# Optimization experiments

Measured on AMD Instinct MI355X. Metric: run time of the kernel, lower is better.

The kernel has to match this reference:

```python
import jax, jax.numpy as jnp
import numpy as np

MESH_SIZE = 0.01
TEMP = 0.001
T = 4096
HID = (16, 16, 16)


def _triangle_mesh():
    g = np.arange(-1.0, 1.0 + 1e-9, MESH_SIZE, dtype=np.float32)  # 201 pts
    A, B = np.meshgrid(g, g, indexing='ij')  # alpha rows, beta cols
    mask = A >= B                             # Preisach triangle alpha >= beta
    return A[mask].astype(np.float32), B[mask].astype(np.float32)  # [N], [N]


def _constrain(v, lo, hi):
    return lo + (hi - lo) * jax.nn.sigmoid(v)


def setup_inputs() -> dict:
    key = jax.random.key(0)
    ks = jax.random.split(key, 12)
    alpha_np, beta_np = _triangle_mesh()
    N = alpha_np.shape[0]  # 20301

    def xavier(k, fan_in, fan_out):
        b = np.sqrt(6.0 / (fan_in + fan_out)).astype(np.float32)
        return jax.random.uniform(k, (fan_in, fan_out), jnp.float32, -b, b)

    dims = (2,) + HID + (1,)
    params = {}
    for i in range(4):
        params[f'w{i+1}'] = xavier(ks[i], dims[i], dims[i + 1])
        params[f'b{i+1}'] = jnp.zeros((dims[i + 1],), jnp.float32)

    bound = np.sqrt(6.0 / (1 + N)).astype(np.float32)  # xavier_uniform on (1,N)
    init_state_raw = jax.random.uniform(ks[10], (N,), jnp.float32, -bound, bound)

    return dict(
        x=jax.random.normal(ks[11], (T,), jnp.float32),
        alpha_raw=jnp.asarray(alpha_np),
        beta_raw=jnp.asarray(beta_np),
        init_state_raw=init_state_raw,
        m_scale_raw=jnp.asarray(1.0, jnp.float32),
        m_offset_raw=jnp.asarray(1.0, jnp.float32),
        h_scale_raw=jnp.asarray(1.0, jnp.float32),
        **params,
    )


def _get_states(x, alpha, beta, s0, temp):
    # Soft Preisach relay: switch up where u>alpha, down where u<beta, else hold.
    def step(s, u):
        up = jax.nn.sigmoid((u - alpha) / temp)
        dn = jax.nn.sigmoid((beta - u) / temp)
        s_new = up - dn + (1.0 - up) * (1.0 - dn) * s
        return s_new, s_new
    _, states = jax.lax.scan(step, s0, x)
    return states  # [T, N]


def reference(x, alpha_raw, beta_raw, init_state_raw,
              w1, b1, w2, b2, w3, b3, w4, b4,
              m_scale_raw, m_offset_raw, h_scale_raw):
    alpha = alpha_raw  # ConstrainedParameter with no bounds -> identity
    beta = beta_raw
    s0 = jnp.tanh(init_state_raw)  # BinaryParameter (soft binary)

    states = _get_states(x, alpha, beta, s0, TEMP)  # [T, N]

    mesh = jnp.stack([alpha, beta], axis=1)  # [N, 2]
    h = jax.nn.relu(mesh @ w1 + b1)
    h = jax.nn.relu(h @ w2 + b2)
    h = jax.nn.relu(h @ w3 + b3)
    density = jax.nn.sigmoid(h @ w4 + b4)  # [N, 1]
    density = density.T  # [1, N]

    m = jnp.sum(density * states, axis=-1) / jnp.sum(density, axis=-1)  # [T]

    m_scale = _constrain(m_scale_raw, 0.0, 10.0)
    m_offset = _constrain(m_offset_raw, -10.0, 10.0)
    h_scale = _constrain(h_scale_raw, 0.0, 10.0)

    out = m_scale * m + m_offset + h_scale * x  # [T]
    return out, density, states
```

## Files before the change

### kernel.cpp

```cpp
#include <hip/hip_runtime.h>
#include <math.h>

#define NM 20301
#define TT 4096
#define NC 16
#define CH 256
#define NBLK 80
#define NWAVE 4
#define NPAR (NBLK*NWAVE)
#define TPH 16
#define NPH (CH / TPH)
#define LOG2E_K 1442.69504f

__device__ __forceinline__ void relay_step(float ka, float kb, float ku,
                                           float& aa, float& bb) {
    float z1 = fminf(ka - ku, 63.f);
    float z2 = fminf(ku - kb, 63.f);
    float e1 = __builtin_amdgcn_exp2f(z1);
    float e2 = __builtin_amdgcn_exp2f(z2);
    float p1 = 1.f + e1, p2 = 1.f + e2;
    float r  = __builtin_amdgcn_rcpf(p1 * p2);
    aa = (e2 - e1) * r;
    bb = (e1 * e2) * r;
}

__device__ __forceinline__ float wave_reduce_sum(float w) {
    #pragma unroll
    for (int off = 32; off > 0; off >>= 1)
        w += __shfl_down(w, off, 64);
    return w;
}

__global__ __launch_bounds__(256) void density_kernel(
    const float* __restrict__ alpha, const float* __restrict__ beta,
    const float* __restrict__ w1, const float* __restrict__ b1,
    const float* __restrict__ w2, const float* __restrict__ b2,
    const float* __restrict__ w3, const float* __restrict__ b3,
    const float* __restrict__ w4, const float* __restrict__ b4,
    float* __restrict__ density_out, float* __restrict__ densum_parts)
{
    int n = blockIdx.x * 256 + threadIdx.x;
    bool valid = n < NM;
    int nn = valid ? n : NM - 1;
    float a = alpha[nn], b = beta[nn];

    float h1[16], h2[16], h3[16];
    #pragma unroll
    for (int j = 0; j < 16; j++) {
        float v = fmaf(a, w1[j], fmaf(b, w1[16 + j], b1[j]));
        h1[j] = fmaxf(v, 0.f);
    }
    #pragma unroll
    for (int j = 0; j < 16; j++) {
        float v = b2[j];
        #pragma unroll
        for (int k = 0; k < 16; k++) v = fmaf(h1[k], w2[k * 16 + j], v);
        h2[j] = fmaxf(v, 0.f);
    }
    #pragma unroll
    for (int j = 0; j < 16; j++) {
        float v = b3[j];
        #pragma unroll
        for (int k = 0; k < 16; k++) v = fmaf(h2[k], w3[k * 16 + j], v);
        h3[j] = fmaxf(v, 0.f);
    }
    float v = b4[0];
    #pragma unroll
    for (int k = 0; k < 16; k++) v = fmaf(h3[k], w4[k], v);
    float d = 1.f / (1.f + __expf(-v));

    if (valid) density_out[n] = d;
    float wsum = wave_reduce_sum(valid ? d : 0.f);
    __shared__ float ws_[NWAVE];
    if ((threadIdx.x & 63) == 0) ws_[threadIdx.x >> 6] = wsum;
    __syncthreads();
    if (threadIdx.x == 0)
        densum_parts[blockIdx.x] = ws_[0] + ws_[1] + ws_[2] + ws_[3];
}

__global__ __launch_bounds__(256) void chunk_compose_kernel(
    const float* __restrict__ x, const float* __restrict__ alpha,
    const float* __restrict__ beta,
    float* __restrict__ Abuf, float* __restrict__ Bbuf)
{
    __shared__ float xs[CH];
    int c = blockIdx.y;
    xs[threadIdx.x] = x[c * CH + threadIdx.x] * LOG2E_K;
    __syncthreads();

    int n = blockIdx.x * 256 + threadIdx.x;
    int nn = (n < NM) ? n : NM - 1;
    float ka = alpha[nn] * LOG2E_K;
    float kb = beta[nn] * LOG2E_K;

    float A = 0.f, B = 1.f;
    #pragma unroll 8
    for (int i = 0; i < CH; i++) {
        float aa, bb;
        relay_step(ka, kb, xs[i], aa, bb);
        A = fmaf(bb, A, aa);
        B *= bb;
    }
    if (n < NM) { Abuf[c * NM + n] = A; Bbuf[c * NM + n] = B; }
}

__global__ __launch_bounds__(256) void chunk_scan_kernel(
    const float* __restrict__ init_raw,
    const float* __restrict__ Abuf, const float* __restrict__ Bbuf,
    float* __restrict__ sstart)
{
    int n = blockIdx.x * 256 + threadIdx.x;
    if (n >= NM) return;
    float s = tanhf(init_raw[n]);
    #pragma unroll
    for (int c = 0; c < NC; c++) {
        sstart[c * NM + n] = s;
        s = fmaf(Bbuf[c * NM + n], s, Abuf[c * NM + n]);
    }
}

__global__ __launch_bounds__(256) void states_kernel(
    const float* __restrict__ x, const float* __restrict__ alpha,
    const float* __restrict__ beta, const float* __restrict__ density,
    const float* __restrict__ sstart,
    float* __restrict__ states, float* __restrict__ partials)
{
    __shared__ float xs[CH];
    __shared__ float tile[NWAVE * 64 * (TPH + 1)];

    int tid = threadIdx.x;
    int c = blockIdx.y;
    xs[tid] = x[c * CH + tid] * LOG2E_K;

    int n = blockIdx.x * 256 + tid;
    bool valid = n < NM;
    int nn = valid ? n : NM - 1;
    float ka = alpha[nn] * LOG2E_K;
    float kb = beta[nn] * LOG2E_K;
    float d  = valid ? density[n] : 0.f;
    float s  = sstart[c * NM + nn];
    __syncthreads();

    int wv = tid >> 6, ln = tid & 63;
    int tl = ln & 15, h = ln >> 4;
    float* wtile = &tile[wv * 64 * (TPH + 1)];
    float* tslot = &wtile[ln * (TPH + 1)];
    float* rowp  = states + (size_t)c * CH * NM + n;
    size_t prow  = (size_t)(blockIdx.x * NWAVE + wv) * TT + c * CH;

    for (int p = 0; p < NPH; p++) {
        #pragma unroll
        for (int j = 0; j < TPH; j++) {
            int i = p * TPH + j;
            float aa, bb;
            relay_step(ka, kb, xs[i], aa, bb);
            s = fmaf(bb, s, aa);
            if (valid) __builtin_nontemporal_store(s, rowp + (size_t)i * NM);
            tslot[j] = d * s;
        }
        asm volatile("s_waitcnt lgkmcnt(0)" ::: "memory");
        float acc = 0.f;
        #pragma unroll
        for (int k = 0; k < TPH; k++)
            acc += wtile[(h * 16 + k) * (TPH + 1) + tl];
        acc += __shfl_xor(acc, 16, 64);
        acc += __shfl_xor(acc, 32, 64);
        if (ln < TPH) partials[prow + p * TPH + ln] = acc;
        asm volatile("s_waitcnt lgkmcnt(0)" ::: "memory");
    }
}

__global__ __launch_bounds__(256) void finalize_kernel(
    const float* __restrict__ x, const float* __restrict__ partials,
    const float* __restrict__ densum_parts,
    const float* __restrict__ msr, const float* __restrict__ mor,
    const float* __restrict__ hsr, float* __restrict__ out)
{
    int t = blockIdx.x * 256 + threadIdx.x;
    if (t >= TT) return;
    float acc = 0.f;
    for (int r = 0; r < NPAR; r++)
        acc += partials[(size_t)r * TT + t];
    float dsum = 0.f;
    for (int bx = 0; bx < NBLK; bx++)
        dsum += densum_parts[bx];
    float sig_ms = 1.f / (1.f + __expf(-msr[0]));
    float sig_mo = 1.f / (1.f + __expf(-mor[0]));
    float sig_hs = 1.f / (1.f + __expf(-hsr[0]));
    float m_scale  = 10.f * sig_ms;
    float m_offset = fmaf(20.f, sig_mo, -10.f);
    float h_scale  = 10.f * sig_hs;
    float m = acc / dsum;
    out[t] = fmaf(m_scale, m, m_offset) + h_scale * x[t];
}

extern "C" void kernel_launch(void* const* d_in, const int* in_sizes, int n_in,
                              void* d_out, int out_size, void* d_ws, size_t ws_size,
                              hipStream_t stream)
{
    const float* x    = (const float*)d_in[0];
    const float* alpha= (const float*)d_in[1];
    const float* beta = (const float*)d_in[2];
    const float* init = (const float*)d_in[3];
    const float* msr  = (const float*)d_in[4];
    const float* mor  = (const float*)d_in[5];
    const float* hsr  = (const float*)d_in[6];
    const float* w1   = (const float*)d_in[7];
    const float* b1   = (const float*)d_in[8];
    const float* w2   = (const float*)d_in[9];
    const float* b2   = (const float*)d_in[10];
    const float* w3   = (const float*)d_in[11];
    const float* b3   = (const float*)d_in[12];
    const float* w4   = (const float*)d_in[13];
    const float* b4   = (const float*)d_in[14];

    float* out     = (float*)d_out;
    float* density = out + TT;
    float* states  = density + NM;

    float* densum_parts = (float*)d_ws;
    float* sstart       = densum_parts + 128;
    float* partials     = sstart + NC * NM;

    float* Abuf = states;
    float* Bbuf = states + (size_t)NC * NM;

    density_kernel<<<dim3(NBLK), dim3(256), 0, stream>>>(
        alpha, beta, w1, b1, w2, b2, w3, b3, w4, b4, density, densum_parts);

    chunk_compose_kernel<<<dim3(NBLK, NC), dim3(256), 0, stream>>>(
        x, alpha, beta, Abuf, Bbuf);

    chunk_scan_kernel<<<dim3(NBLK), dim3(256), 0, stream>>>(
        init, Abuf, Bbuf, sstart);

    states_kernel<<<dim3(NBLK, NC), dim3(256), 0, stream>>>(
        x, alpha, beta, density, sstart, states, partials);

    finalize_kernel<<<dim3(TT / 256), dim3(256), 0, stream>>>(
        x, partials, densum_parts, msr, mor, hsr, out);
}
```

Measured before the change: 512.4 us.

## Stage states through LDS and emit 16-byte aligned vector stores

The states kernel now writes each step's relay state into a per-wave LDS tile laid out with a row-dependent shift. It then reads the tile back so each lane holds four consecutive neurons and stores them to global memory as float4. The shift handles NM not being a multiple of 4, so rows start at different alignments; edge lanes fall back to scalar stores, and partial tail waves keep the original per-step scalar stores. The density-weighted partial sums are recomputed from the same float4 reads with per-lane density registers and a 16-lane shuffle reduction. The goal is to replace many strided 4-byte stores with wide coalesced ones, at the cost of more LDS traffic and index arithmetic, and the old nontemporal store hint is dropped.

```diff
diff --git a/kernel.cpp b/kernel.cpp
--- a/kernel.cpp
+++ b/kernel.cpp
@@ -11,6 +11,7 @@
 #define TPH 16
 #define NPH (CH / TPH)
 #define LOG2E_K 1442.69504f
+#define SBASE_MOD4 1
 
 __device__ __forceinline__ void relay_step(float ka, float kb, float ku,
                                            float& aa, float& bb) {
@@ -126,7 +127,7 @@
     float* __restrict__ states, float* __restrict__ partials)
 {
     __shared__ float xs[CH];
-    __shared__ float tile[NWAVE * 64 * (TPH + 1)];
+    __shared__ __align__(16) float tile[NWAVE * TPH * 68];
 
     int tid = threadIdx.x;
     int c = blockIdx.y;
@@ -137,16 +138,30 @@
     int nn = valid ? n : NM - 1;
     float ka = alpha[nn] * LOG2E_K;
     float kb = beta[nn] * LOG2E_K;
-    float d  = valid ? density[n] : 0.f;
     float s  = sstart[c * NM + nn];
     __syncthreads();
 
     int wv = tid >> 6, ln = tid & 63;
-    int tl = ln & 15, h = ln >> 4;
-    float* wtile = &tile[wv * 64 * (TPH + 1)];
-    float* tslot = &wtile[ln * (TPH + 1)];
-    float* rowp  = states + (size_t)c * CH * NM + n;
-    size_t prow  = (size_t)(blockIdx.x * NWAVE + wv) * TT + c * CH;
+    int tg = ln >> 4,  li = ln & 15;
+    int m   = (tg + 1) & 3;
+    int off = (4 - m) & 3;
+    int A   = m ? 4 : 0;
+
+    float* wtile = &tile[wv * TPH * 68];
+    int  nb   = blockIdx.x * 256 + wv * 64;
+    bool fast = (nb + 64 <= NM);
+
+    bool lane_x4 = (off == 0) || (li < 15);
+    int  e0 = (off == 0) ? 4 * li : off + 4 * li;
+    float dreg[4];
+    #pragma unroll
+    for (int k = 0; k < 4; k++) {
+        int e  = lane_x4 ? (e0 + k) : ((k < off) ? k : 60 + k);
+        int nk = nb + e;
+        dreg[k] = (nk < NM) ? density[nk] : 0.f;
+    }
+
+    size_t prow = (size_t)(blockIdx.x * NWAVE + wv) * TT + c * CH;
 
     for (int p = 0; p < NPH; p++) {
         #pragma unroll
@@ -155,17 +170,40 @@
             float aa, bb;
             relay_step(ka, kb, xs[i], aa, bb);
             s = fmaf(bb, s, aa);
-            if (valid) __builtin_nontemporal_store(s, rowp + (size_t)i * NM);
-            tslot[j] = d * s;
+            wtile[j * 68 + (((j & 3) + 1) & 3) + ln] = s;
+            if (!fast && valid)
+                states[(size_t)(c * CH + i) * NM + n] = s;
         }
         asm volatile("s_waitcnt lgkmcnt(0)" ::: "memory");
-        float acc = 0.f;
-        #pragma unroll
-        for (int k = 0; k < TPH; k++)
-            acc += wtile[(h * 16 + k) * (TPH + 1) + tl];
-        acc += __shfl_xor(acc, 16, 64);
-        acc += __shfl_xor(acc, 32, 64);
-        if (ln < TPH) partials[prow + p * TPH + ln] = acc;
+
+        #pragma unroll
+        for (int r = 0; r < 4; r++) {
+            int j = tg + 4 * r;
+            int t = c * CH + p * TPH + j;
+            size_t g0 = (size_t)t * NM + nb;
+            float v0, v1, v2, v3;
+            if (lane_x4) {
+                const float4 vv = *(const float4*)&wtile[j * 68 + A + 4 * li];
+                v0 = vv.x; v1 = vv.y; v2 = vv.z; v3 = vv.w;
+                if (fast) *(float4*)(states + g0 + e0) = vv;
+            } else {
+                #pragma unroll
+                for (int k = 0; k < 4; k++) {
+                    int e = (k < off) ? k : 60 + k;
+                    float sv = wtile[j * 68 + m + e];
+                    if (k == 0) v0 = sv; else if (k == 1) v1 = sv;
+                    else if (k == 2) v2 = sv; else v3 = sv;
+                    if (fast) states[g0 + e] = sv;
+                }
+            }
+            float q = fmaf(v0, dreg[0], fmaf(v1, dreg[1],
+                      fmaf(v2, dreg[2], v3 * dreg[3])));
+            q += __shfl_xor(q, 1);
+            q += __shfl_xor(q, 2);
+            q += __shfl_xor(q, 4);
+            q += __shfl_xor(q, 8);
+            if (li == 0) partials[prow + p * TPH + j] = q;
+        }
         asm volatile("s_waitcnt lgkmcnt(0)" ::: "memory");
     }
 }
```

Result: faster. 498.6 us (-2.7%).
